# Kernel optimization log

Measured on AMD Instinct MI355X. Metric: run time of the kernel, lower is better.

The kernel has to match this reference:

```python
import jax, jax.numpy as jnp
import numpy as np

NEG_INF_DIAG = 1000000.0

def setup_inputs() -> dict:
    key = jax.random.key(0)
    k1, k2, k3 = jax.random.split(key, 3)
    B, N, S, D = 64, 32, 256, 128
    return {
        "query_embeddings": jax.random.normal(k1, (B, N, D), dtype=jnp.float32),
        "doc_embeddings": jax.random.normal(k2, (B, S, D), dtype=jnp.float32),
        "neg_doc_embeddings": jax.random.normal(k3, (B, S, D), dtype=jnp.float32),
    }

def _maxsim(q, d):
    # q: (b, n, dim), d: (b, s, dim) -> (b,) sum over n of max over s of q.d
    return jnp.einsum('bnd,bsd->bns', q, d).max(axis=2).sum(axis=1)

def reference(query_embeddings, doc_embeddings, neg_doc_embeddings):
    pos_scores = _maxsim(query_embeddings, doc_embeddings)
    neg_scores = _maxsim(query_embeddings, neg_doc_embeddings)
    loss = jax.nn.softplus(neg_scores - pos_scores).mean()

    # in-batch term: scores[b, c] = MaxSim(query b, doc c)
    scores = jnp.einsum('bnd,csd->bcns', query_embeddings, doc_embeddings).max(axis=3).sum(axis=2)  # (B, B)
    pos = jnp.diagonal(scores)
    B = scores.shape[0]
    neg = (scores - jnp.eye(B, dtype=scores.dtype) * NEG_INF_DIAG).max(axis=1)
    loss = loss + jax.nn.softplus(neg - pos).mean()
    return loss / 2
```

## Files before the change

### kernel.cpp

```cpp
#include <hip/hip_runtime.h>
#include <hip/hip_bf16.h>

#define B_SZ 64

typedef __attribute__((ext_vector_type(8))) short bf16x8;
typedef __attribute__((ext_vector_type(4))) float f32x4;

static __device__ __forceinline__ unsigned short f2bf(float f) {
    __hip_bfloat16 h = __float2bfloat16(f);
    return *reinterpret_cast<unsigned short*>(&h);
}

static __device__ __forceinline__ bf16x8 cvt_frag(const float* __restrict__ src) {
    float4 a = reinterpret_cast<const float4*>(src)[0];
    float4 b = reinterpret_cast<const float4*>(src)[1];
    union { bf16x8 v; unsigned short u[8]; } t;
    t.u[0] = f2bf(a.x); t.u[1] = f2bf(a.y); t.u[2] = f2bf(a.z); t.u[3] = f2bf(a.w);
    t.u[4] = f2bf(b.x); t.u[5] = f2bf(b.y); t.u[6] = f2bf(b.z); t.u[7] = f2bf(b.w);
    return t.v;
}

#define MFMA(A, Bv, C) __builtin_amdgcn_mfma_f32_16x16x32_bf16(A, Bv, C, 0, 0, 0)

__global__ __launch_bounds__(256, 2) void maxsim_kernel(const float* __restrict__ q,
                                                        const float* __restrict__ dd,
                                                        const float* __restrict__ nd,
                                                        float* __restrict__ scores) {
    const int idx = blockIdx.x, tid = threadIdx.x;
    const int wave = tid >> 6, lane = tid & 63;
    const int l15 = lane & 15, l4 = lane >> 4;

    __shared__ bf16x8 docB[4096];

    int b0, b1, ccol;
    const float* docf;
    if (idx < 512) {
        const int c = idx >> 3, g = idx & 7;
        b0 = g * 8 + wave * 2; b1 = b0 + 1; ccol = c;
        docf = dd + (size_t)c * 32768;
    } else {
        b0 = b1 = idx - 512; ccol = B_SZ;
        docf = nd + (size_t)b0 * 32768;
    }

    bf16x8 Af[2][4][2];
    #pragma unroll
    for (int kk = 0; kk < 4; ++kk)
        #pragma unroll
        for (int mt = 0; mt < 2; ++mt) {
            const int off = (mt * 16 + l15) * 128 + kk * 32 + l4 * 8;
            Af[0][kk][mt] = cvt_frag(q + (size_t)b0 * 4096 + off);
            Af[1][kk][mt] = cvt_frag(q + (size_t)b1 * 4096 + off);
        }

    {
        const float* dsrc = docf + wave * 8192;
        #pragma unroll
        for (int f = 0; f < 16; ++f) {
            const int s_local = f * 4 + l4;
            const int kc = l15;
            bf16x8 v = cvt_frag(dsrc + s_local * 128 + kc * 8);
            const int logical = wave * 1024 + (kc >> 2) * 256 + (s_local >> 4) * 64
                                + (kc & 3) * 16 + (s_local & 15);
            docB[logical ^ ((kc >> 2) << 1)] = v;
        }
    }
    __syncthreads();

    float rmax[2][2][4];
    #pragma unroll
    for (int qi = 0; qi < 2; ++qi)
        #pragma unroll
        for (int mt = 0; mt < 2; ++mt)
            #pragma unroll
            for (int r = 0; r < 4; ++r) rmax[qi][mt][r] = -3.0e38f;

    #pragma unroll
    for (int i = 0; i < 4; ++i) {
        const int ch = (wave + i) & 3;
        f32x4 acc[2][2][4] = {};
        #pragma unroll
        for (int kk = 0; kk < 4; ++kk) {
            const int rbase = ch * 1024 + kk * 256 + (lane ^ (kk << 1));
            #pragma unroll
            for (int nt = 0; nt < 4; ++nt) {
                bf16x8 Bv = docB[rbase + nt * 64];
                acc[0][0][nt] = MFMA(Af[0][kk][0], Bv, acc[0][0][nt]);
                acc[0][1][nt] = MFMA(Af[0][kk][1], Bv, acc[0][1][nt]);
                acc[1][0][nt] = MFMA(Af[1][kk][0], Bv, acc[1][0][nt]);
                acc[1][1][nt] = MFMA(Af[1][kk][1], Bv, acc[1][1][nt]);
            }
        }
        #pragma unroll
        for (int qi = 0; qi < 2; ++qi)
            #pragma unroll
            for (int mt = 0; mt < 2; ++mt)
                #pragma unroll
                for (int r = 0; r < 4; ++r)
                    rmax[qi][mt][r] = fmaxf(rmax[qi][mt][r],
                        fmaxf(fmaxf(acc[qi][mt][0][r], acc[qi][mt][1][r]),
                              fmaxf(acc[qi][mt][2][r], acc[qi][mt][3][r])));
    }

    #pragma unroll
    for (int qi = 0; qi < 2; ++qi) {
        float part = 0.0f;
        #pragma unroll
        for (int mt = 0; mt < 2; ++mt)
            #pragma unroll
            for (int r = 0; r < 4; ++r) {
                float m = rmax[qi][mt][r];
                m = fmaxf(m, __shfl_xor(m, 1, 64));
                m = fmaxf(m, __shfl_xor(m, 2, 64));
                m = fmaxf(m, __shfl_xor(m, 4, 64));
                m = fmaxf(m, __shfl_xor(m, 8, 64));
                part += m;
            }
        part += __shfl_xor(part, 16, 64);
        part += __shfl_xor(part, 32, 64);
        const int b = qi ? b1 : b0;
        if (lane == 0 && (idx < 512 ? true : (wave == 0 && qi == 0)))
            scores[(size_t)b * 65 + ccol] = part;
    }
}

static __device__ __forceinline__ float softplusf(float x) {
    return fmaxf(x, 0.0f) + log1pf(expf(-fabsf(x)));
}

__global__ __launch_bounds__(64) void loss_kernel(const float* __restrict__ scores,
                                                  float* __restrict__ out) {
    const int b = threadIdx.x;
    const float* row = scores + b * 65;
    const float pos  = row[b];
    const float negq = row[64];
    float nib = -1e30f;
    #pragma unroll
    for (int c = 0; c < B_SZ; ++c) {
        float v = row[c] - ((c == b) ? 1000000.0f : 0.0f);
        nib = fmaxf(nib, v);
    }
    float t = softplusf(negq - pos) + softplusf(nib - pos);
    t += __shfl_xor(t, 1, 64);
    t += __shfl_xor(t, 2, 64);
    t += __shfl_xor(t, 4, 64);
    t += __shfl_xor(t, 8, 64);
    t += __shfl_xor(t, 16, 64);
    t += __shfl_xor(t, 32, 64);
    if (b == 0) out[0] = t * (0.5f / 64.0f);
}

extern "C" void kernel_launch(void* const* d_in, const int* in_sizes, int n_in,
                              void* d_out, int out_size, void* d_ws, size_t ws_size,
                              hipStream_t stream) {
    const float* q  = (const float*)d_in[0];
    const float* dd = (const float*)d_in[1];
    const float* nd = (const float*)d_in[2];
    float* out = (float*)d_out;

    float* scores = (float*)d_ws;

    maxsim_kernel<<<512 + B_SZ, 256, 0, stream>>>(q, dd, nd, scores);

    loss_kernel<<<1, 64, 0, stream>>>(scores, out);
}
```

Before: 109.1 us.

## Pre-convert embeddings to bf16 fragment layout in separate pass before maxsim

Adds a pre-pass kernel that converts queries and docs from fp32 to bf16 once and writes them in MFMA fragment order to workspace. The main kernel then loads fragments directly, with no per-block fp32 conversion. Before, each doc was converted eight times, once per block that read it. Doc staging now goes through a half-size shared buffer in two phases, and launch bounds rise to three blocks per CU. The cost is an extra kernel launch and a round trip of the bf16 data through global memory.

```diff
diff --git a/kernel.cpp b/kernel.cpp
--- a/kernel.cpp
+++ b/kernel.cpp
@@ -22,50 +22,66 @@
 
 #define MFMA(A, Bv, C) __builtin_amdgcn_mfma_f32_16x16x32_bf16(A, Bv, C, 0, 0, 0)
 
-__global__ __launch_bounds__(256, 2) void maxsim_kernel(const float* __restrict__ q,
-                                                        const float* __restrict__ dd,
-                                                        const float* __restrict__ nd,
+__global__ __launch_bounds__(256) void cvt_permute(const float* __restrict__ q,
+                                                   const float* __restrict__ dd,
+                                                   const float* __restrict__ nd,
+                                                   unsigned short* __restrict__ DP,
+                                                   unsigned short* __restrict__ QP) {
+    const int blk = blockIdx.x, tid = threadIdx.x;
+    if (blk < 2048) {
+        const int o = blk * 256 + tid;
+        const int doc = o >> 12;
+        const int u = o & 4095;
+        const int ln = u & 63, nt = (u >> 6) & 3, kk = (u >> 8) & 3, ch = u >> 10;
+        const int s  = ch * 64 + nt * 16 + (ln & 15);
+        const int k0 = kk * 32 + (ln >> 4) * 8;
+        const float* src = ((doc < 64) ? (dd + (size_t)doc * 32768)
+                                       : (nd + (size_t)(doc - 64) * 32768)) + s * 128 + k0;
+        reinterpret_cast<bf16x8*>(DP)[o] = cvt_frag(src);
+    } else {
+        const int g = (blk - 2048) * 256 + tid;
+        const int b = g >> 9, u = g & 511;
+        const int ln = u & 63, mt = (u >> 6) & 1, kk = u >> 7;
+        const int n  = mt * 16 + (ln & 15);
+        const int k0 = kk * 32 + (ln >> 4) * 8;
+        reinterpret_cast<bf16x8*>(QP)[g] = cvt_frag(q + (size_t)b * 4096 + n * 128 + k0);
+    }
+}
+
+__global__ __launch_bounds__(256, 3) void maxsim_kernel(const unsigned short* __restrict__ QP,
+                                                        const unsigned short* __restrict__ DP,
                                                         float* __restrict__ scores) {
     const int idx = blockIdx.x, tid = threadIdx.x;
     const int wave = tid >> 6, lane = tid & 63;
-    const int l15 = lane & 15, l4 = lane >> 4;
 
-    __shared__ bf16x8 docB[4096];
+    __shared__ bf16x8 docB[2048];
 
-    int b0, b1, ccol;
-    const float* docf;
-    if (idx < 512) {
-        const int c = idx >> 3, g = idx & 7;
-        b0 = g * 8 + wave * 2; b1 = b0 + 1; ccol = c;
-        docf = dd + (size_t)c * 32768;
+    int b0, b1, ccol, dcc;
+    const bool isNeg = (idx >= 512);
+    if (!isNeg) {
+        const int c = idx >> 3, bg = idx & 7;
+        b0 = bg * 8 + wave * 2; b1 = b0 + 1;
+        ccol = c; dcc = c;
     } else {
-        b0 = b1 = idx - 512; ccol = B_SZ;
-        docf = nd + (size_t)b0 * 32768;
+        b0 = b1 = idx - 512;
+        ccol = B_SZ; dcc = 64 + b0;
     }
 
+    const bf16x8* QP8 = reinterpret_cast<const bf16x8*>(QP);
+    const bf16x8* DP8 = reinterpret_cast<const bf16x8*>(DP);
+
     bf16x8 Af[2][4][2];
-    #pragma unroll
-    for (int kk = 0; kk < 4; ++kk)
+    {
+        const bf16x8* q0 = QP8 + (size_t)b0 * 512 + lane;
+        const bf16x8* q1 = QP8 + (size_t)b1 * 512 + lane;
         #pragma unroll
-        for (int mt = 0; mt < 2; ++mt) {
-            const int off = (mt * 16 + l15) * 128 + kk * 32 + l4 * 8;
-            Af[0][kk][mt] = cvt_frag(q + (size_t)b0 * 4096 + off);
-            Af[1][kk][mt] = cvt_frag(q + (size_t)b1 * 4096 + off);
-        }
-
-    {
-        const float* dsrc = docf + wave * 8192;
-        #pragma unroll
-        for (int f = 0; f < 16; ++f) {
-            const int s_local = f * 4 + l4;
-            const int kc = l15;
-            bf16x8 v = cvt_frag(dsrc + s_local * 128 + kc * 8);
-            const int logical = wave * 1024 + (kc >> 2) * 256 + (s_local >> 4) * 64
-                                + (kc & 3) * 16 + (s_local & 15);
-            docB[logical ^ ((kc >> 2) << 1)] = v;
+        for (int kk = 0; kk < 4; ++kk) {
+            Af[0][kk][0] = q0[kk * 128];
+            Af[0][kk][1] = q0[kk * 128 + 64];
+            Af[1][kk][0] = q1[kk * 128];
+            Af[1][kk][1] = q1[kk * 128 + 64];
         }
     }
-    __syncthreads();
 
     float rmax[2][2][4];
     #pragma unroll
@@ -75,31 +91,43 @@
             #pragma unroll
             for (int r = 0; r < 4; ++r) rmax[qi][mt][r] = -3.0e38f;
 
+    const bf16x8* dbase = DP8 + (size_t)dcc * 4096;
+
     #pragma unroll
-    for (int i = 0; i < 4; ++i) {
-        const int ch = (wave + i) & 3;
-        f32x4 acc[2][2][4] = {};
+    for (int h = 0; h < 2; ++h) {
+        if (h) __syncthreads();
+        {
+            const bf16x8* src = dbase + h * 2048;
+            #pragma unroll
+            for (int f = 0; f < 8; ++f)
+                docB[f * 256 + tid] = src[f * 256 + tid];
+        }
+        __syncthreads();
+
         #pragma unroll
-        for (int kk = 0; kk < 4; ++kk) {
-            const int rbase = ch * 1024 + kk * 256 + (lane ^ (kk << 1));
+        for (int cc = 0; cc < 2; ++cc) {
+            f32x4 acc[2][2][4] = {};
             #pragma unroll
-            for (int nt = 0; nt < 4; ++nt) {
-                bf16x8 Bv = docB[rbase + nt * 64];
-                acc[0][0][nt] = MFMA(Af[0][kk][0], Bv, acc[0][0][nt]);
-                acc[0][1][nt] = MFMA(Af[0][kk][1], Bv, acc[0][1][nt]);
-                acc[1][0][nt] = MFMA(Af[1][kk][0], Bv, acc[1][0][nt]);
-                acc[1][1][nt] = MFMA(Af[1][kk][1], Bv, acc[1][1][nt]);
+            for (int kk = 0; kk < 4; ++kk) {
+                #pragma unroll
+                for (int nt = 0; nt < 4; ++nt) {
+                    bf16x8 Bv = docB[cc * 1024 + kk * 256 + nt * 64 + lane];
+                    acc[0][0][nt] = MFMA(Af[0][kk][0], Bv, acc[0][0][nt]);
+                    acc[0][1][nt] = MFMA(Af[0][kk][1], Bv, acc[0][1][nt]);
+                    acc[1][0][nt] = MFMA(Af[1][kk][0], Bv, acc[1][0][nt]);
+                    acc[1][1][nt] = MFMA(Af[1][kk][1], Bv, acc[1][1][nt]);
+                }
             }
+            #pragma unroll
+            for (int qi = 0; qi < 2; ++qi)
+                #pragma unroll
+                for (int mt = 0; mt < 2; ++mt)
+                    #pragma unroll
+                    for (int r = 0; r < 4; ++r)
+                        rmax[qi][mt][r] = fmaxf(rmax[qi][mt][r],
+                            fmaxf(fmaxf(acc[qi][mt][0][r], acc[qi][mt][1][r]),
+                                  fmaxf(acc[qi][mt][2][r], acc[qi][mt][3][r])));
         }
-        #pragma unroll
-        for (int qi = 0; qi < 2; ++qi)
-            #pragma unroll
-            for (int mt = 0; mt < 2; ++mt)
-                #pragma unroll
-                for (int r = 0; r < 4; ++r)
-                    rmax[qi][mt][r] = fmaxf(rmax[qi][mt][r],
-                        fmaxf(fmaxf(acc[qi][mt][0][r], acc[qi][mt][1][r]),
-                              fmaxf(acc[qi][mt][2][r], acc[qi][mt][3][r])));
     }
 
     #pragma unroll
@@ -119,7 +147,7 @@
         part += __shfl_xor(part, 16, 64);
         part += __shfl_xor(part, 32, 64);
         const int b = qi ? b1 : b0;
-        if (lane == 0 && (idx < 512 ? true : (wave == 0 && qi == 0)))
+        if (lane == 0 && (!isNeg || (wave == 0 && qi == 0)))
             scores[(size_t)b * 65 + ccol] = part;
     }
 }
@@ -158,9 +186,13 @@
     const float* nd = (const float*)d_in[2];
     float* out = (float*)d_out;
 
-    float* scores = (float*)d_ws;
+    unsigned short* DP = (unsigned short*)d_ws;
+    unsigned short* QP = DP + (size_t)128 * 32768;
+    float* scores = (float*)(QP + (size_t)64 * 4096);
 
-    maxsim_kernel<<<512 + B_SZ, 256, 0, stream>>>(q, dd, nd, scores);
+    cvt_permute<<<2176, 256, 0, stream>>>(q, dd, nd, DP, QP);
+
+    maxsim_kernel<<<512 + B_SZ, 256, 0, stream>>>(QP, DP, scores);
 
     loss_kernel<<<1, 64, 0, stream>>>(scores, out);
 }
```

Measured after the change: 91.57 us. 16.1% less time.
